# Kernel optimization log

Hardware: AMD Instinct MI355X
Metric: run time of the kernel (lower is better)

## Reference

```python
import jax, jax.numpy as jnp
import numpy as np

B, L, D = 4, 2048, 2048
H, KVH, HD = 16, 4, 128          # num_heads, num_kv_heads, head_dim = D // H
M = 16                           # mem_tokens
BASE = 10000.0
EPS = 1.1920929e-07              # torch F.rms_norm default eps = fp32 machine eps


def _rms_norm(x):
    # normalize over last dim, no learned weight (matches F.rms_norm(x, (hd,)))
    return x * jax.lax.rsqrt(jnp.mean(x * x, axis=-1, keepdims=True) + EPS)


def _apply_rotary(x, cos, sin):
    # x: [B, h, T, HD]; cos/sin: [1, 1, T, HD//2]
    half = x.shape[-1] // 2
    x1, x2 = x[..., :half], x[..., half:]
    return jnp.concatenate([x1 * cos + x2 * sin, -x1 * sin + x2 * cos], axis=-1)


def setup_inputs() -> dict:
    key = jax.random.key(0)
    k0, k1, k2, k3, k4 = jax.random.split(key, 5)
    kv_dim = KVH * HD
    s = 0.02
    return {
        "x": jax.random.normal(k0, (B, L, D), dtype=jnp.float32),
        "Wq": jax.random.normal(k1, (D, D), dtype=jnp.float32) * s,
        "Wk": jax.random.normal(k2, (kv_dim, D), dtype=jnp.float32) * s,
        "Wv": jax.random.normal(k3, (kv_dim, D), dtype=jnp.float32) * s,
        "Wproj": jax.random.normal(k4, (D, D), dtype=jnp.float32) * s,
        "q_gain": jnp.full((H,), 1.0, dtype=jnp.float32),
    }


def reference(x, Wq, Wk, Wv, Wproj, q_gain):
    Bx, Lx, Dx = x.shape
    # QKV projections (Linear: x @ W.T), split into heads -> [B, h, L, HD]
    q = (x @ Wq.T).reshape(Bx, Lx, H, HD).transpose(0, 2, 1, 3)
    k = (x @ Wk.T).reshape(Bx, Lx, KVH, HD).transpose(0, 2, 1, 3)
    v = (x @ Wv.T).reshape(Bx, Lx, KVH, HD).transpose(0, 2, 1, 3)
    # QK RMSNorm
    q = _rms_norm(q)
    k = _rms_norm(k)
    # RoPE on the non-memory tokens only
    T = Lx - M
    inv_freq = 1.0 / BASE ** (jnp.arange(0, HD, 2, dtype=jnp.float32) / HD)
    freqs = jnp.outer(jnp.arange(T, dtype=jnp.float32), inv_freq)  # [T, HD//2]
    cos = jnp.cos(freqs)[None, None]
    sin = jnp.sin(freqs)[None, None]
    q = jnp.concatenate([q[:, :, :M], _apply_rotary(q[:, :, M:], cos, sin)], axis=2)
    k = jnp.concatenate([k[:, :, :M], _apply_rotary(k[:, :, M:], cos, sin)], axis=2)
    # per-head gain on q
    q = q * q_gain[None, :, None, None]
    # GQA attention: group q heads by kv head (matches repeat_interleave ordering)
    rep = H // KVH
    qg = q.reshape(Bx, KVH, rep, Lx, HD)
    scale = 1.0 / np.sqrt(HD).astype(np.float32)
    scores = jnp.einsum('bgrqd,bgkd->bgrqk', qg, k) * scale  # [B, KVH, rep, L, L]
    causal = jnp.tril(jnp.ones((Lx, Lx), dtype=bool))
    scores = jnp.where(causal, scores, -jnp.inf)
    p = jax.nn.softmax(scores, axis=-1)
    y = jnp.einsum('bgrqk,bgkd->bgrqd', p, v)                # [B, KVH, rep, L, HD]
    y = y.reshape(Bx, H, Lx, HD).transpose(0, 2, 1, 3).reshape(Bx, Lx, Dx)
    return y @ Wproj.T
```

## Files before the change

### kernel.cpp

```cpp
#include <hip/hip_runtime.h>
#include <stdint.h>

typedef unsigned short u16;
typedef short s8v __attribute__((ext_vector_type(8)));
typedef float f4v __attribute__((ext_vector_type(4)));
typedef float f16v __attribute__((ext_vector_type(16)));

typedef __attribute__((address_space(1))) char gchar;
typedef __attribute__((address_space(3))) char lchar;

static __device__ __forceinline__ u16 f2bf(float f) {
  uint32_t x = __float_as_uint(f);
  x += 0x7fffu + ((x >> 16) & 1u);
  return (u16)(x >> 16);
}
static __device__ __forceinline__ float bf2f(u16 u) {
  return __uint_as_float(((uint32_t)u) << 16);
}
static __device__ __forceinline__ void gload_lds16(const void* g, void* l) {
  __builtin_amdgcn_global_load_lds((gchar*)(uintptr_t)g,
                                   (lchar*)(uint32_t)(uintptr_t)l, 16, 0, 0);
}

__global__ __launch_bounds__(256) void cvt_bf16(const float4* __restrict__ src,
                                                uint2* __restrict__ dst, int n4) {
  int i = blockIdx.x * 256 + threadIdx.x;
  int st = gridDim.x * 256;
  for (; i < n4; i += st) {
    float4 v = src[i];
    uint2 o;
    o.x = (uint32_t)f2bf(v.x) | ((uint32_t)f2bf(v.y) << 16);
    o.y = (uint32_t)f2bf(v.z) | ((uint32_t)f2bf(v.w) << 16);
    dst[i] = o;
  }
}

__global__ __launch_bounds__(256) void cvt_bf16_w(const float4* __restrict__ s0,
                                                  const float4* __restrict__ s1,
                                                  const float4* __restrict__ s2,
                                                  const float4* __restrict__ s3,
                                                  uint2* __restrict__ dst) {
  int i = blockIdx.x * 256 + threadIdx.x;
  int st = gridDim.x * 256;
  for (; i < 2621440; i += st) {
    const float4* s;
    int off;
    if (i < 1048576)      { s = s0; off = i; }
    else if (i < 1310720) { s = s1; off = i - 1048576; }
    else if (i < 1572864) { s = s2; off = i - 1310720; }
    else                  { s = s3; off = i - 1572864; }
    float4 v = s[off];
    uint2 o;
    o.x = (uint32_t)f2bf(v.x) | ((uint32_t)f2bf(v.y) << 16);
    o.y = (uint32_t)f2bf(v.z) | ((uint32_t)f2bf(v.w) << 16);
    dst[i] = o;
  }
}

__global__ __launch_bounds__(256) void rope_table(float* __restrict__ tc,
                                                  float* __restrict__ ts) {
  int i = blockIdx.x * 256 + threadIdx.x;
  if (i >= 2032 * 64) return;
  int t = i >> 6, f = i & 63;
  float invf = 1.0f / powf(10000.0f, (float)f * (1.0f / 64.0f));
  float ang = (float)t * invf;
  float s, c;
  sincosf(ang, &s, &c);
  tc[i] = c;
  ts[i] = s;
}

template <int MODE>
__global__ __launch_bounds__(512, 2) void gemm_nt(
    const u16* __restrict__ A, const u16* __restrict__ W0,
    const u16* __restrict__ W1, const u16* __restrict__ W2,
    u16* __restrict__ O0, u16* __restrict__ O1, u16* __restrict__ O2,
    float* __restrict__ OF) {
  __shared__ u16 lA[4][256 * 32];
  __shared__ u16 lB[4][128 * 32];
  const int tid = threadIdx.x;
  const int lane = tid & 63, wid = tid >> 6;
  const int wr = wid >> 1, wc = wid & 1;
  const int l15 = lane & 15, l4 = lane >> 4;

  const int NB = (MODE == 0) ? 24 : 16;
  const int nwg = gridDim.x;
  const int bid = blockIdx.x;
  const int swz = (bid & 7) * (nwg >> 3) + (bid >> 3);
  const int bm = swz / NB, bn = swz % NB;
  const int m0 = bm * 256;

  const u16* Wt;
  int n0r;
  if constexpr (MODE == 0) {
    if (bn < 16)      { Wt = W0; n0r = bn * 128; }
    else if (bn < 20) { Wt = W1; n0r = (bn - 16) * 128; }
    else              { Wt = W2; n0r = (bn - 20) * 128; }
  } else {
    Wt = W0; n0r = bn * 128;
  }

  auto stage = [&](int kt, int bsel) {
    const int kb = kt * 32;
#pragma unroll
    for (int c = 0; c < 2; ++c) {
      int cidx = tid + c * 512;
      int p = cidx >> 3, q = cidx & 7;
      int qp = q ^ (p & 7);
      int r = 2 * p + (qp >> 2), k8 = qp & 3;
      gload_lds16(A + (size_t)(m0 + r) * 2048 + kb + k8 * 8, &lA[bsel][cidx * 8]);
    }
    {
      int cidx = tid;
      int p = cidx >> 3, q = cidx & 7;
      int qp = q ^ (p & 7);
      int r = 2 * p + (qp >> 2), k8 = qp & 3;
      gload_lds16(Wt + (size_t)(n0r + r) * 2048 + kb + k8 * 8, &lB[bsel][cidx * 8]);
    }
  };
  auto swzoff = [&](int fr, int s) {
    return (fr >> 1) * 64 + (((s + ((fr & 1) << 2)) ^ ((fr >> 1) & 7)) << 3);
  };

  const f4v Z4 = {0.f, 0.f, 0.f, 0.f};
  f4v acc[4][4];
#pragma unroll
  for (int i = 0; i < 4; i++)
#pragma unroll
    for (int j = 0; j < 4; j++) acc[i][j] = Z4;

  stage(0, 0);
  stage(1, 1);
  stage(2, 2);

  const int NT = 64;
  for (int t = 0; t < NT; ++t) {
    const int cur = t & 3;
    asm volatile("s_waitcnt lgkmcnt(0)" ::: "memory");
    __builtin_amdgcn_sched_barrier(0);
    asm volatile("s_barrier" ::: "memory");
    if (t + 3 < NT) {
      stage(t + 3, (t + 3) & 3);
      asm volatile("s_waitcnt vmcnt(9)" ::: "memory");
    } else if (t == NT - 3) {
      asm volatile("s_waitcnt vmcnt(6)" ::: "memory");
    } else if (t == NT - 2) {
      asm volatile("s_waitcnt vmcnt(3)" ::: "memory");
    } else {
      asm volatile("s_waitcnt vmcnt(0)" ::: "memory");
    }
    asm volatile("s_barrier" ::: "memory");

    const u16* pa = &lA[cur][0];
    const u16* pb = &lB[cur][0];
    s8v afrg[4], bfrg[4];
#pragma unroll
    for (int i = 0; i < 4; ++i)
      afrg[i] = *(const s8v*)&pa[swzoff(wr * 64 + i * 16 + l15, l4)];
#pragma unroll
    for (int j = 0; j < 4; ++j)
      bfrg[j] = *(const s8v*)&pb[swzoff(wc * 64 + j * 16 + l15, l4)];
    __builtin_amdgcn_s_setprio(1);
#pragma unroll
    for (int i = 0; i < 4; ++i)
#pragma unroll
      for (int j = 0; j < 4; ++j)
        acc[i][j] = __builtin_amdgcn_mfma_f32_16x16x32_bf16(afrg[i], bfrg[j], acc[i][j], 0, 0, 0);
    __builtin_amdgcn_s_setprio(0);
  }

  const int ncol0 = bn * 128 + wc * 64;
  if constexpr (MODE == 0) {
    const int colg = ncol0;
    u16* Ob; int hh, HX;
    if (colg < 2048)      { Ob = O0; hh = colg >> 7;          HX = 16; }
    else if (colg < 2560) { Ob = O1; hh = (colg - 2048) >> 7; HX = 4; }
    else                  { Ob = O2; hh = (colg - 2560) >> 7; HX = 4; }
    const int d0 = colg & 127;
#pragma unroll
    for (int i = 0; i < 4; i++)
#pragma unroll
      for (int r = 0; r < 4; r++) {
        int m = m0 + wr * 64 + i * 16 + l4 * 4 + r;
        int b = m >> 11, l = m & 2047;
        size_t base = ((size_t)(b * HX + hh) * 2048 + l) * 128 + d0;
#pragma unroll
        for (int j = 0; j < 4; j++)
          Ob[base + j * 16 + l15] = f2bf(acc[i][j][r]);
      }
  } else {
#pragma unroll
    for (int i = 0; i < 4; i++)
#pragma unroll
      for (int r = 0; r < 4; r++) {
        int m = m0 + wr * 64 + i * 16 + l4 * 4 + r;
#pragma unroll
        for (int j = 0; j < 4; j++)
          OF[(size_t)m * 2048 + ncol0 + j * 16 + l15] = acc[i][j][r];
      }
  }
}

__global__ __launch_bounds__(256) void norm_rope(u16* __restrict__ buf,
                                                 const float* __restrict__ gain,
                                                 const float* __restrict__ tc,
                                                 const float* __restrict__ ts) {
  const int lane = threadIdx.x & 63;
  const int gw = blockIdx.x * 4 + (threadIdx.x >> 6);
  const int nw = gridDim.x * 4;
  for (int row = gw; row < 163840; row += nw) {
    int l = row & 2047;
    u16* p = buf + (size_t)row * 128;
    float x1 = bf2f(p[lane]);
    float x2 = bf2f(p[lane + 64]);
    float ss = x1 * x1 + x2 * x2;
#pragma unroll
    for (int off = 32; off > 0; off >>= 1) ss += __shfl_xor(ss, off, 64);
    float r = rsqrtf(ss * (1.0f / 128.0f) + 1.1920929e-07f);
    x1 *= r; x2 *= r;
    if (l >= 16) {
      int t = l - 16;
      float c = tc[t * 64 + lane], s = ts[t * 64 + lane];
      float o1 = x1 * c + x2 * s;
      float o2 = -x1 * s + x2 * c;
      x1 = o1; x2 = o2;
    }
    if (row < 131072) {
      float g = gain[(row >> 11) & 15];
      x1 *= g; x2 *= g;
    }
    p[lane] = f2bf(x1);
    p[lane + 64] = f2bf(x2);
  }
}

__global__ __launch_bounds__(256) void transpose_v(const u16* __restrict__ v,
                                                   u16* __restrict__ vt) {
  __shared__ u16 t[64][64];
  const int l0 = blockIdx.x * 64, d0 = blockIdx.y * 64, bg = blockIdx.z;
  const int tid = threadIdx.x;
#pragma unroll
  for (int it = 0; it < 2; ++it) {
    int lin = it * 256 + tid;
    int r = lin >> 3, cb = lin & 7;
    s8v val = *(const s8v*)&v[((bg * 2048 + l0 + r) * 128) + d0 + cb * 8];
    *(s8v*)&t[r][(cb ^ (r & 7)) * 8] = val;
  }
  __syncthreads();
#pragma unroll
  for (int it = 0; it < 2; ++it) {
    int lin = it * 256 + tid;
    int r2 = lin >> 3, c2 = (lin & 7) * 8;
    s8v o;
#pragma unroll
    for (int j = 0; j < 8; ++j) {
      int rr = c2 + j, cc = r2;
      o[j] = (short)t[rr][(cc & 7) + 8 * ((cc >> 3) ^ (rr & 7))];
    }
    *(s8v*)&vt[((bg * 128 + d0 + r2) * 2048) + l0 + c2] = o;
  }
}

__global__ __launch_bounds__(256, 2) void attn(const u16* __restrict__ q,
                                               const u16* __restrict__ k,
                                               const u16* __restrict__ vt,
                                               u16* __restrict__ y) {
  __shared__ u16 lK[2][64 * 128];
  __shared__ u16 lVT[2][128 * 64];
  const int tid = threadIdx.x;
  const int lane = tid & 63, wid = tid >> 6;
  const int l31 = lane & 31, hi = lane >> 5;

  const int db = (int)blockIdx.y * 32 + (int)blockIdx.x;
  const int half = db >> 8, rem = db & 255;
  const int bg = (rem & 7) + 8 * half;
  const int pairi = rem >> 3;
  const int b = bg >> 2, g = bg & 3;
  const int h = g * 4 + wid;

  const u16* qh = q + (size_t)(b * 16 + h) * 2048 * 128;
  const u16* kb0 = k + (size_t)(b * 4 + g) * 2048 * 128;
  const u16* vtb0 = vt + (size_t)(b * 4 + g) * 128 * 2048;
  const float scale = 0.08838834764831845f;

  auto stage = [&](int t, int bufsel) {
    const int kv0 = t * 64;
#pragma unroll
    for (int it = 0; it < 4; ++it) {
      int lin = it * 256 + tid;
      int kj = lin >> 4, s = lin & 15;
      gload_lds16(kb0 + (size_t)(kv0 + kj) * 128 + ((s ^ (kj & 7)) * 8),
                  &lK[bufsel][lin * 8]);
    }
#pragma unroll
    for (int it = 0; it < 4; ++it) {
      int lin = it * 256 + tid;
      int d = lin >> 3, s = lin & 7;
      gload_lds16(vtb0 + (size_t)d * 2048 + kv0 + ((s ^ (d & 7)) * 8),
                  &lVT[bufsel][lin * 8]);
    }
  };

  for (int ph = 0; ph < 2; ++ph) {
    const int qt = ph ? (63 - pairi) : pairi;
    const int q0 = qt * 32;
    const int nt = (q0 >> 6) + 1;
    const int qabs = q0 + l31;

    s8v qf[8];
#pragma unroll
    for (int ks = 0; ks < 8; ++ks)
      qf[ks] = *(const s8v*)&qh[(q0 + l31) * 128 + ks * 16 + hi * 8];

    f16v yacc[4];
#pragma unroll
    for (int j = 0; j < 4; ++j)
#pragma unroll
      for (int r = 0; r < 16; ++r) yacc[j][r] = 0.f;
    float mrow = -1e30f, lrow = 0.f;

    stage(0, 0);
    __syncthreads();

    for (int t = 0; t < nt; ++t) {
      const int cur = t & 1;
      if (t + 1 < nt) stage(t + 1, cur ^ 1);
      const int kv0 = t * 64;

      f16v s0a, s1a;
#pragma unroll
      for (int r = 0; r < 16; ++r) { s0a[r] = 0.f; s1a[r] = 0.f; }
      __builtin_amdgcn_s_setprio(1);
#pragma unroll
      for (int ks = 0; ks < 8; ++ks) {
        const int slot = (2 * ks + hi) ^ (l31 & 7);
        s8v kf0 = *(const s8v*)&lK[cur][(l31)*128 + slot * 8];
        s8v kf1 = *(const s8v*)&lK[cur][(32 + l31) * 128 + slot * 8];
        s0a = __builtin_amdgcn_mfma_f32_32x32x16_bf16(kf0, qf[ks], s0a, 0, 0, 0);
        s1a = __builtin_amdgcn_mfma_f32_32x32x16_bf16(kf1, qf[ks], s1a, 0, 0, 0);
      }
      __builtin_amdgcn_s_setprio(0);

      const bool last = (t == nt - 1);
      float p0[16], p1[16];
      float pmax = -1e30f;
#pragma unroll
      for (int r = 0; r < 16; ++r) {
        const int kvloc = (r & 3) + 8 * (r >> 2) + 4 * hi;
        float v0 = s0a[r] * scale;
        float v1 = s1a[r] * scale;
        if (last) {
          if (kv0 + kvloc > qabs) v0 = -1e30f;
          if (kv0 + 32 + kvloc > qabs) v1 = -1e30f;
        }
        p0[r] = v0; p1[r] = v1;
        pmax = fmaxf(pmax, fmaxf(v0, v1));
      }
      pmax = fmaxf(pmax, __shfl_xor(pmax, 32, 64));

      if (!__all(pmax - mrow <= 8.0f)) {
        float mnew = fmaxf(mrow, pmax);
        float corr = __expf(mrow - mnew);
#pragma unroll
        for (int r = 0; r < 16; ++r) {
          const int qloc = (r & 3) + 8 * (r >> 2) + 4 * hi;
          float cb = __shfl(corr, qloc, 64);
          yacc[0][r] *= cb; yacc[1][r] *= cb; yacc[2][r] *= cb; yacc[3][r] *= cb;
        }
        lrow *= corr;
        mrow = mnew;
      }

      float ps = 0.f;
#pragma unroll
      for (int r = 0; r < 16; ++r) {
        float e0 = bf2f(f2bf(__expf(p0[r] - mrow)));
        float e1 = bf2f(f2bf(__expf(p1[r] - mrow)));
        p0[r] = e0; p1[r] = e1;
        ps += e0 + e1;
      }
      ps += __shfl_xor(ps, 32, 64);
      lrow += ps;

      __builtin_amdgcn_s_setprio(1);
#pragma unroll
      for (int ks = 0; ks < 4; ++ks) {
        const float* pc = (ks < 2) ? p0 : p1;
        const int rb = 8 * (ks & 1);
        uint32_t A0 = (uint32_t)f2bf(pc[rb + 0]) | ((uint32_t)f2bf(pc[rb + 1]) << 16);
        uint32_t A1 = (uint32_t)f2bf(pc[rb + 2]) | ((uint32_t)f2bf(pc[rb + 3]) << 16);
        uint32_t B0 = (uint32_t)f2bf(pc[rb + 4]) | ((uint32_t)f2bf(pc[rb + 5]) << 16);
        uint32_t B1 = (uint32_t)f2bf(pc[rb + 6]) | ((uint32_t)f2bf(pc[rb + 7]) << 16);
        uint32_t t0 = hi ? A0 : B0;
        uint32_t t1 = hi ? A1 : B1;
        uint32_t r0 = (uint32_t)__shfl_xor((int)t0, 32, 64);
        uint32_t r1 = (uint32_t)__shfl_xor((int)t1, 32, 64);
        union { uint32_t u[4]; s8v v; } uu;
        uu.u[0] = hi ? r0 : A0;
        uu.u[1] = hi ? r1 : A1;
        uu.u[2] = hi ? B0 : r0;
        uu.u[3] = hi ? B1 : r1;
#pragma unroll
        for (int jd = 0; jd < 4; ++jd) {
          const int rowd = 32 * jd + l31;
          const int slot = (2 * ks + hi) ^ (l31 & 7);
          s8v vf = *(const s8v*)&lVT[cur][rowd * 64 + slot * 8];
          yacc[jd] = __builtin_amdgcn_mfma_f32_32x32x16_bf16(uu.v, vf, yacc[jd], 0, 0, 0);
        }
      }
      __builtin_amdgcn_s_setprio(0);
      __syncthreads();
    }

    float inv = 1.0f / lrow;
#pragma unroll
    for (int r = 0; r < 16; ++r) {
      const int qloc = (r & 3) + 8 * (r >> 2) + 4 * hi;
      float ib = __shfl(inv, qloc, 64);
      const int qrow = q0 + qloc;
      size_t base = ((size_t)(b * 2048 + qrow)) * 2048 + h * 128 + l31;
#pragma unroll
      for (int jd = 0; jd < 4; ++jd)
        y[base + 32 * jd] = f2bf(yacc[jd][r] * ib);
    }
  }
}

extern "C" void kernel_launch(void* const* d_in, const int* in_sizes, int n_in,
                              void* d_out, int out_size, void* d_ws, size_t ws_size,
                              hipStream_t stream) {
  const float* x  = (const float*)d_in[0];
  const float* Wq = (const float*)d_in[1];
  const float* Wk = (const float*)d_in[2];
  const float* Wv = (const float*)d_in[3];
  const float* Wp = (const float*)d_in[4];
  const float* qg = (const float*)d_in[5];
  float* out = (float*)d_out;

  char* ws = (char*)d_ws;
  size_t off = 0;
  auto alloc = [&](size_t bytes) {
    void* p = ws + off;
    off += (bytes + 255) & ~(size_t)255;
    return p;
  };
  u16* x_bf  = (u16*)alloc((size_t)8192 * 2048 * 2);
  u16* wq_bf = (u16*)alloc((size_t)2048 * 2048 * 2);
  u16* wk_bf = (u16*)alloc((size_t)512 * 2048 * 2);
  u16* wv_bf = (u16*)alloc((size_t)512 * 2048 * 2);
  u16* wp_bf = (u16*)alloc((size_t)2048 * 2048 * 2);
  u16* q_bf  = (u16*)alloc((size_t)4 * 16 * 2048 * 128 * 2);
  u16* k_bf  = (u16*)alloc((size_t)4 * 4 * 2048 * 128 * 2);
  u16* v_bf  = (u16*)alloc((size_t)4 * 4 * 2048 * 128 * 2);
  float* tab = (float*)alloc((size_t)2032 * 64 * 2 * 4);
  u16* y_bf  = x_bf;
  u16* vt_bf = wq_bf;

  cvt_bf16<<<2048, 256, 0, stream>>>((const float4*)x, (uint2*)x_bf, 8192 * 2048 / 4);
  cvt_bf16_w<<<1024, 256, 0, stream>>>((const float4*)Wq, (const float4*)Wk,
                                       (const float4*)Wv, (const float4*)Wp,
                                       (uint2*)wq_bf);
  rope_table<<<(2032 * 64 + 255) / 256, 256, 0, stream>>>(tab, tab + 2032 * 64);

  gemm_nt<0><<<dim3(768), 512, 0, stream>>>(x_bf, wq_bf, wk_bf, wv_bf,
                                            q_bf, k_bf, v_bf, nullptr);
  norm_rope<<<2048, 256, 0, stream>>>(q_bf, qg, tab, tab + 2032 * 64);
  transpose_v<<<dim3(32, 2, 16), 256, 0, stream>>>(v_bf, vt_bf);
  attn<<<dim3(32, 16), 256, 0, stream>>>(q_bf, k_bf, vt_bf, y_bf);
  gemm_nt<1><<<dim3(512), 512, 0, stream>>>(y_bf, wp_bf, nullptr, nullptr,
                                            nullptr, nullptr, nullptr, out);
}
```

Measured before the change: 376.3 us.

## Switch GEMM pipeline to double-buffered BK=64 tiles with simpler LDS swizzle

The NT GEMM's K tile doubles from 32 to 64 and its LDS pipeline drops from four stages to two (one prefetch in flight). The swizzle is rewritten for 64-wide rows, and each iteration runs two MFMA k-substeps. This halves the number of barrier and waitcnt rounds per tile and keeps the LDS footprint the same. In exchange, less prefetch depth is available to hide global load latency.

Measured after the change: 358.2 us. 1.05x faster.

```diff
diff --git a/kernel.cpp b/kernel.cpp
--- a/kernel.cpp
+++ b/kernel.cpp
@@ -76,8 +76,8 @@
     const u16* __restrict__ W1, const u16* __restrict__ W2,
     u16* __restrict__ O0, u16* __restrict__ O1, u16* __restrict__ O2,
     float* __restrict__ OF) {
-  __shared__ u16 lA[4][256 * 32];
-  __shared__ u16 lB[4][128 * 32];
+  __shared__ u16 lA[2][256 * 64];
+  __shared__ u16 lB[2][128 * 64];
   const int tid = threadIdx.x;
   const int lane = tid & 63, wid = tid >> 6;
   const int wr = wid >> 1, wc = wid & 1;
@@ -101,25 +101,24 @@
   }
 
   auto stage = [&](int kt, int bsel) {
-    const int kb = kt * 32;
+    const int kb = kt * 64;
+#pragma unroll
+    for (int c = 0; c < 4; ++c) {
+      int cidx = tid + c * 512;
+      int r = cidx >> 3, s = cidx & 7;
+      gload_lds16(A + (size_t)(m0 + r) * 2048 + kb + ((s ^ (r & 7)) * 8),
+                  &lA[bsel][cidx * 8]);
+    }
 #pragma unroll
     for (int c = 0; c < 2; ++c) {
       int cidx = tid + c * 512;
-      int p = cidx >> 3, q = cidx & 7;
-      int qp = q ^ (p & 7);
-      int r = 2 * p + (qp >> 2), k8 = qp & 3;
-      gload_lds16(A + (size_t)(m0 + r) * 2048 + kb + k8 * 8, &lA[bsel][cidx * 8]);
-    }
-    {
-      int cidx = tid;
-      int p = cidx >> 3, q = cidx & 7;
-      int qp = q ^ (p & 7);
-      int r = 2 * p + (qp >> 2), k8 = qp & 3;
-      gload_lds16(Wt + (size_t)(n0r + r) * 2048 + kb + k8 * 8, &lB[bsel][cidx * 8]);
+      int r = cidx >> 3, s = cidx & 7;
+      gload_lds16(Wt + (size_t)(n0r + r) * 2048 + kb + ((s ^ (r & 7)) * 8),
+                  &lB[bsel][cidx * 8]);
     }
   };
   auto swzoff = [&](int fr, int s) {
-    return (fr >> 1) * 64 + (((s + ((fr & 1) << 2)) ^ ((fr >> 1) & 7)) << 3);
+    return fr * 64 + (((s) ^ (fr & 7)) << 3);
   };
 
   const f4v Z4 = {0.f, 0.f, 0.f, 0.f};
@@ -130,22 +129,16 @@
     for (int j = 0; j < 4; j++) acc[i][j] = Z4;
 
   stage(0, 0);
-  stage(1, 1);
-  stage(2, 2);
-
-  const int NT = 64;
+
+  const int NT = 32;
   for (int t = 0; t < NT; ++t) {
-    const int cur = t & 3;
+    const int cur = t & 1;
     asm volatile("s_waitcnt lgkmcnt(0)" ::: "memory");
     __builtin_amdgcn_sched_barrier(0);
     asm volatile("s_barrier" ::: "memory");
-    if (t + 3 < NT) {
-      stage(t + 3, (t + 3) & 3);
-      asm volatile("s_waitcnt vmcnt(9)" ::: "memory");
-    } else if (t == NT - 3) {
+    if (t + 1 < NT) {
+      stage(t + 1, cur ^ 1);
       asm volatile("s_waitcnt vmcnt(6)" ::: "memory");
-    } else if (t == NT - 2) {
-      asm volatile("s_waitcnt vmcnt(3)" ::: "memory");
     } else {
       asm volatile("s_waitcnt vmcnt(0)" ::: "memory");
     }
@@ -153,20 +146,23 @@
 
     const u16* pa = &lA[cur][0];
     const u16* pb = &lB[cur][0];
-    s8v afrg[4], bfrg[4];
-#pragma unroll
-    for (int i = 0; i < 4; ++i)
-      afrg[i] = *(const s8v*)&pa[swzoff(wr * 64 + i * 16 + l15, l4)];
-#pragma unroll
-    for (int j = 0; j < 4; ++j)
-      bfrg[j] = *(const s8v*)&pb[swzoff(wc * 64 + j * 16 + l15, l4)];
-    __builtin_amdgcn_s_setprio(1);
-#pragma unroll
-    for (int i = 0; i < 4; ++i)
+#pragma unroll
+    for (int ks = 0; ks < 2; ++ks) {
+      s8v afrg[4], bfrg[4];
+#pragma unroll
+      for (int i = 0; i < 4; ++i)
+        afrg[i] = *(const s8v*)&pa[swzoff(wr * 64 + i * 16 + l15, ks * 4 + l4)];
 #pragma unroll
       for (int j = 0; j < 4; ++j)
-        acc[i][j] = __builtin_amdgcn_mfma_f32_16x16x32_bf16(afrg[i], bfrg[j], acc[i][j], 0, 0, 0);
-    __builtin_amdgcn_s_setprio(0);
+        bfrg[j] = *(const s8v*)&pb[swzoff(wc * 64 + j * 16 + l15, ks * 4 + l4)];
+      __builtin_amdgcn_s_setprio(1);
+#pragma unroll
+      for (int i = 0; i < 4; ++i)
+#pragma unroll
+        for (int j = 0; j < 4; ++j)
+          acc[i][j] = __builtin_amdgcn_mfma_f32_16x16x32_bf16(afrg[i], bfrg[j], acc[i][j], 0, 0, 0);
+      __builtin_amdgcn_s_setprio(0);
+    }
   }
 
   const int ncol0 = bn * 128 + wc * 64;
```
